# Optimization experiments

Measured on AMD Instinct MI355X. Metric: run time of the kernel, lower is better.

## Reference

```python
import jax, jax.numpy as jnp
import numpy as np


def conv3x3(x, w):
    # x: [B,C,H,W], w: [O,I,3,3], stride 1, pad 1, no bias
    return jax.lax.conv_general_dilated(
        x, w, window_strides=(1, 1), padding=[(1, 1), (1, 1)],
        dimension_numbers=("NCHW", "OIHW", "NCHW"))


def deform_conv2d(x, offset, w):
    """torchvision-style DeformConv2d: k=3, stride=1, pad=1, dilation=1,
    1 offset group, no bias. x:[B,C,H,W], offset:[B,18,H,W] (dy,dx pairs
    per kernel tap, k = kh*3+kw), w:[O,C,3,3]. Zero padding outside."""
    B, C, H, W = x.shape
    K = 9
    dy = offset[:, 0::2]  # [B,9,H,W]
    dx = offset[:, 1::2]
    kh = (jnp.arange(K) // 3 - 1).astype(x.dtype)[None, :, None, None]
    kw = (jnp.arange(K) % 3 - 1).astype(x.dtype)[None, :, None, None]
    hh = jnp.arange(H, dtype=x.dtype)[None, None, :, None]
    ww = jnp.arange(W, dtype=x.dtype)[None, None, None, :]
    py = hh + kh + dy  # sampling y coord, [B,9,H,W]
    px = ww + kw + dx
    y0 = jnp.floor(py)
    x0 = jnp.floor(px)
    wy = py - y0
    wx = px - x0
    x_hwc = jnp.transpose(x, (0, 2, 3, 1))  # [B,H,W,C]
    b_idx = jnp.arange(B)[:, None, None, None]

    def gather(yi, xi):
        valid = (yi >= 0) & (yi <= H - 1) & (xi >= 0) & (xi <= W - 1)
        yc = jnp.clip(yi, 0, H - 1).astype(jnp.int32)
        xc = jnp.clip(xi, 0, W - 1).astype(jnp.int32)
        v = x_hwc[b_idx, yc, xc]  # [B,9,H,W,C]
        return v * valid[..., None].astype(x.dtype)

    v00 = gather(y0, x0)
    v01 = gather(y0, x0 + 1)
    v10 = gather(y0 + 1, x0)
    v11 = gather(y0 + 1, x0 + 1)
    wy = wy[..., None]
    wx = wx[..., None]
    sampled = (v00 * (1 - wy) * (1 - wx) + v01 * (1 - wy) * wx
               + v10 * wy * (1 - wx) + v11 * wy * wx)  # [B,9,H,W,C]
    wk = w.reshape(w.shape[0], w.shape[1], K)  # [O,C,9]
    return jnp.einsum("bkhwc,ock->bohw", sampled, wk)


def setup_inputs() -> dict:
    key = jax.random.key(0)
    ks = jax.random.split(key, 6)
    B, C, H, W = 2, 128, 128, 128
    s = 0.05  # small init so learned offsets stay in a realistic range
    return {
        "input_features": jax.random.normal(ks[0], (B, C, H, W), jnp.float32),
        "reference_features": jax.random.normal(ks[1], (B, C, H, W), jnp.float32),
        "w_est1": jax.random.normal(ks[2], (C, 2 * C, 3, 3), jnp.float32) * s,
        "w_est2": jax.random.normal(ks[3], (C, C, 3, 3), jnp.float32) * s,
        "w_off": jax.random.normal(ks[4], (18, C, 3, 3), jnp.float32) * s,
        "w_def": jax.random.normal(ks[5], (C, C, 3, 3), jnp.float32) * s,
    }


def reference(input_features, reference_features, w_est1, w_est2, w_off, w_def):
    # concat input+reference features along channel dim
    feat = jnp.concatenate([input_features, reference_features], axis=1)  # [B,2C,H,W]
    # dynamic offset estimator: 2-layer 3x3 conv stack 2C->C->C with ReLU
    est = jax.nn.relu(conv3x3(feat, w_est1))
    est = jax.nn.relu(conv3x3(est, w_est2))
    # offset head: C -> 2*9 offsets per pixel
    offset = conv3x3(est, w_off)  # [B,18,H,W]
    # deformable conv over the reference features
    return deform_conv2d(reference_features, offset, w_def)
```

## Files before the change

kernel.cpp:

```cpp
#include <hip/hip_runtime.h>

typedef _Float16 f16;
typedef __attribute__((ext_vector_type(8))) _Float16 f16x8;
typedef __attribute__((ext_vector_type(4))) float f32x4;


__device__ __forceinline__ void g2l16(const void* g, void* l) {
  __builtin_amdgcn_global_load_lds((const __attribute__((address_space(1))) void*)g,
                                   (__attribute__((address_space(3))) void*)l, 16, 0, 0);
}

__device__ __forceinline__ void pack_conv(const float* __restrict__ src, f16* __restrict__ dst,
                                          long idx, int C) {
  int ci3 = idx & 7;
  int g = (idx >> 3) & 3;
  long t = idx >> 5;
  int o = (int)(t & 63); t >>= 6;
  int kx = (int)(t % 3); t /= 3;
  int nb = (int)(t & 1); t >>= 1;
  int nkc = C >> 5;
  int cc = (int)(t % nkc);
  int ky = (int)(t / nkc);
  int og = nb * 64 + o;
  int c = (cc << 5) + ((g ^ ((o >> 1) & 3)) << 3) + ci3;
  dst[idx] = (f16)src[(((size_t)og * C + c) * 3 + ky) * 3 + kx];
}

__device__ __forceinline__ void halo_zero(f16* __restrict__ buf, long e) {
  int c = (int)(e & 127);
  long t = e >> 7;
  int b = (int)(t / 516);
  int p = (int)(t % 516);
  int y, x;
  if (p < 130)      { y = 0;   x = p; }
  else if (p < 260) { y = 129; x = p - 130; }
  else if (p < 388) { x = 0;   y = p - 259; }
  else              { x = 129; y = p - 387; }
  buf[((size_t)(b * 130 + y) * 130 + x) * 128 + c] = (f16)0.f;
}

__global__ __launch_bounds__(256) void init_k(const float* __restrict__ x, const float* __restrict__ ref,
                                              const float* __restrict__ w1, const float* __restrict__ w2,
                                              const float* __restrict__ woff, const float* __restrict__ wdef,
                                              f16* __restrict__ W1p, f16* __restrict__ W2p,
                                              f16* __restrict__ Woffp, f16* __restrict__ Wdefp,
                                              f16* __restrict__ xP, f16* __restrict__ refP,
                                              f16* __restrict__ est1, f16* __restrict__ est2) {
  __shared__ __align__(16) f16 T[64][40];
  int tid = threadIdx.x;
  if (blockIdx.x < 4096) {
    int bi = blockIdx.x;
    int row = bi & 255, wseg = (bi >> 8) & 1, chunk = bi >> 9;
    int b = row >> 7, h = row & 127;
    int w0 = wseg * 64;
    const float* src = (chunk < 4) ? x : ref;
    f16* dstp = (chunk < 4) ? xP : refP;
    int c0 = (chunk & 3) * 32;
#pragma unroll
    for (int i = 0; i < 2; ++i) {
      int idx = tid + i * 256;
      int c = idx >> 4, g = idx & 15;
      const float4 v = *(const float4*)(src + (((size_t)(b * 128 + c0 + c)) * 128 + h) * 128 + w0 + g * 4);
      T[g * 4 + 0][c] = (f16)v.x;
      T[g * 4 + 1][c] = (f16)v.y;
      T[g * 4 + 2][c] = (f16)v.z;
      T[g * 4 + 3][c] = (f16)v.w;
    }
    __syncthreads();
    int w = tid >> 2, g = tid & 3;
    f16x8 o = *(const f16x8*)&T[w][g * 8];
    *(f16x8*)(dstp + ((size_t)(b * 130 + h + 1) * 130 + w0 + w + 1) * 128 + c0 + g * 8) = o;
    return;
  }
  long idx = (long)(blockIdx.x - 4096) * 256 + tid;
  if (idx < 294912) { pack_conv(w1, W1p, idx, 256); return; }
  idx -= 294912;
  if (idx < 147456) { pack_conv(w2, W2p, idx, 128); return; }
  idx -= 147456;
  if (idx < 36864) {
    int ci3 = (int)(idx & 7);
    int g = (int)((idx >> 3) & 3);
    int o = (int)((idx >> 5) & 31);
    int t2 = (int)(idx >> 10);
    int kx = t2 % 3; t2 /= 3;
    int cc = t2 & 3, ky = t2 >> 2;
    int c = (cc << 5) + ((g ^ ((o >> 1) & 3)) << 3) + ci3;
    Woffp[idx] = (o < 18) ? (f16)woff[(((size_t)o * 128 + c) * 3 + ky) * 3 + kx] : (f16)0.f;
    return;
  }
  idx -= 36864;
  if (idx < 147456) {
    int j = (int)(idx & 7);
    int ln = (int)((idx >> 3) & 63);
    int ofr = (int)((idx >> 9) & 7);
    int cc = (int)((idx >> 12) & 3);
    int t = (int)(idx >> 14);
    int o = ofr * 16 + (ln & 15);
    int c = cc * 32 + (ln >> 4) * 8 + j;
    Wdefp[idx] = (f16)wdef[(((size_t)o * 128 + c) * 3 + t / 3) * 3 + t % 3];
    return;
  }
  idx -= 147456;
  if (idx < 132096) { halo_zero(xP, idx); return; }
  idx -= 132096;
  if (idx < 132096) { halo_zero(refP, idx); return; }
  idx -= 132096;
  if (idx < 132096) { halo_zero(est1, idx); return; }
  idx -= 132096;
  if (idx < 132096) halo_zero(est2, idx);
}

template <int NKC>
__global__ __launch_bounds__(256, 3) void conv_k(const f16* __restrict__ src0,
                                                 const f16* __restrict__ src1,
                                                 const f16* __restrict__ Wp,
                                                 f16* __restrict__ dst) {
  constexpr int S = 3 * NKC;
  const int j = blockIdx.x;
  const int xcd = j & 7, ji = j >> 3;
  const int row = xcd * 32 + (ji & 31);
  const int nb = ji >> 5;
  const int b = row >> 7, h = row & 127;
  __shared__ __align__(16) f16 As[2][130][32];
  __shared__ __align__(16) f16 Bs[2][3][64][32];
  const int tid = threadIdx.x;
  const int lane = tid & 63, wave = tid >> 6;
  const int l16 = lane & 15, quad = lane >> 4;
  const int wmB = wave * 32;
  f32x4 acc[2][4] = {};

  auto stage = [&](int s, int buf) {
    int ky = s / NKC, cc = s % NKC;
    const f16* sp = (NKC == 8 && cc >= 4) ? src1 : src0;
    int c0 = (NKC == 8 ? (cc & 3) : cc) * 32;
    const f16* abase = sp + ((size_t)(b * 130 + h + ky) * 130) * 128 + c0;
#pragma unroll
    for (int rr = 0; rr < 2; ++rr) {
      int ch = rr * 256 + tid;
      int xx = ch >> 2, g = ch & 3;
      g2l16(abase + (size_t)xx * 128 + ((g ^ ((xx >> 1) & 3)) << 3),
            (char*)&As[buf][0][0] + ch * 16);
    }
    if (tid < 8) {
      int ch = 512 + tid;
      int xx = ch >> 2, g = ch & 3;
      g2l16(abase + (size_t)xx * 128 + ((g ^ ((xx >> 1) & 3)) << 3),
            (char*)&As[buf][0][0] + ch * 16);
    }
    const f16* bbase = Wp + (size_t)((ky * NKC + cc) * 2 + nb) * (3 * 64 * 32);
#pragma unroll
    for (int rr = 0; rr < 3; ++rr) {
      int ch = rr * 256 + tid;
      g2l16(bbase + (size_t)ch * 8, (char*)&Bs[buf][0][0][0] + ch * 16);
    }
  };

  stage(0, 0);
  __syncthreads();
  for (int s = 0; s < S; ++s) {
    if (s + 1 < S) stage(s + 1, (s + 1) & 1);
    const int buf = s & 1;
#pragma unroll
    for (int kx = 0; kx < 3; ++kx) {
      f16x8 bf[4];
#pragma unroll
      for (int j2 = 0; j2 < 4; ++j2) {
        int o = j2 * 16 + l16;
        bf[j2] = *(const f16x8*)&Bs[buf][kx][o][(quad ^ ((o >> 1) & 3)) << 3];
      }
#pragma unroll
      for (int i = 0; i < 2; ++i) {
        int xx = wmB + i * 16 + l16 + kx;
        f16x8 a = *(const f16x8*)&As[buf][xx][(quad ^ ((xx >> 1) & 3)) << 3];
#pragma unroll
        for (int j2 = 0; j2 < 4; ++j2)
          acc[i][j2] = __builtin_amdgcn_mfma_f32_16x16x32_f16(a, bf[j2], acc[i][j2], 0, 0, 0);
      }
    }
    __syncthreads();
  }
#pragma unroll
  for (int i = 0; i < 2; ++i)
#pragma unroll
    for (int j2 = 0; j2 < 4; ++j2) {
      int o = nb * 64 + j2 * 16 + l16;
#pragma unroll
      for (int rr = 0; rr < 4; ++rr) {
        int m = wmB + i * 16 + quad * 4 + rr;
        float v = fmaxf(acc[i][j2][rr], 0.f);
        dst[((size_t)(b * 130 + h + 1) * 130 + m + 1) * 128 + o] = (f16)v;
      }
    }
}

__global__ __launch_bounds__(256, 3) void conv_off_k(const f16* __restrict__ src,
                                                     const f16* __restrict__ Wp,
                                                     float* __restrict__ dst) {
  const int j = blockIdx.x;
  const int row = (j & 7) * 32 + (j >> 3);
  const int b = row >> 7, h = row & 127;
  __shared__ __align__(16) f16 As[2][130][32];
  __shared__ __align__(16) f16 Bs[2][3][32][32];
  const int tid = threadIdx.x;
  const int lane = tid & 63, wave = tid >> 6;
  const int l16 = lane & 15, quad = lane >> 4;
  const int wmB = wave * 32;
  f32x4 acc[2][2] = {};

  auto stage = [&](int s, int buf) {
    int ky = s >> 2, cc = s & 3;
    const f16* abase = src + ((size_t)(b * 130 + h + ky) * 130) * 128 + cc * 32;
#pragma unroll
    for (int rr = 0; rr < 2; ++rr) {
      int ch = rr * 256 + tid;
      int xx = ch >> 2, g = ch & 3;
      g2l16(abase + (size_t)xx * 128 + ((g ^ ((xx >> 1) & 3)) << 3),
            (char*)&As[buf][0][0] + ch * 16);
    }
    if (tid < 8) {
      int ch = 512 + tid;
      int xx = ch >> 2, g = ch & 3;
      g2l16(abase + (size_t)xx * 128 + ((g ^ ((xx >> 1) & 3)) << 3),
            (char*)&As[buf][0][0] + ch * 16);
    }
    const f16* bbase = Wp + (size_t)(ky * 4 + cc) * (3 * 32 * 32);
    {
      g2l16(bbase + (size_t)tid * 8, (char*)&Bs[buf][0][0][0] + tid * 16);
      if (tid < 128) {
        int ch = 256 + tid;
        g2l16(bbase + (size_t)ch * 8, (char*)&Bs[buf][0][0][0] + ch * 16);
      }
    }
  };

  stage(0, 0);
  __syncthreads();
  for (int s = 0; s < 12; ++s) {
    if (s + 1 < 12) stage(s + 1, (s + 1) & 1);
    const int buf = s & 1;
#pragma unroll
    for (int kx = 0; kx < 3; ++kx) {
      f16x8 bf[2];
#pragma unroll
      for (int j2 = 0; j2 < 2; ++j2) {
        int o = j2 * 16 + l16;
        bf[j2] = *(const f16x8*)&Bs[buf][kx][o][(quad ^ ((o >> 1) & 3)) << 3];
      }
#pragma unroll
      for (int i = 0; i < 2; ++i) {
        int xx = wmB + i * 16 + l16 + kx;
        f16x8 a = *(const f16x8*)&As[buf][xx][(quad ^ ((xx >> 1) & 3)) << 3];
#pragma unroll
        for (int j2 = 0; j2 < 2; ++j2)
          acc[i][j2] = __builtin_amdgcn_mfma_f32_16x16x32_f16(a, bf[j2], acc[i][j2], 0, 0, 0);
      }
    }
    __syncthreads();
  }
#pragma unroll
  for (int i = 0; i < 2; ++i)
#pragma unroll
    for (int j2 = 0; j2 < 2; ++j2)
#pragma unroll
      for (int rr = 0; rr < 4; ++rr) {
        int m = wmB + i * 16 + quad * 4 + rr;
        int o = j2 * 16 + l16;
        dst[((size_t)row * 128 + m) * 32 + o] = acc[i][j2][rr];
      }
}

__global__ __launch_bounds__(256, 3) void deform_k(const f16* __restrict__ refP,
                                                   const float* __restrict__ offb,
                                                   const f16* __restrict__ Wdefp,
                                                   float* __restrict__ out) {
  const int j = blockIdx.x;
  const int xcd = j & 7, ji = j >> 3;
  const int row = xcd * 32 + (ji & 31);
  const int tile = ji >> 5;
  const int b = row >> 7, h = row & 127;
  __shared__ __align__(16) f16 Ss[2][64][128];
  __shared__ int4 meta[9][64];
  const int tid = threadIdx.x;
  const int lane = tid & 63, wave = tid >> 6;
  const int l16 = lane & 15, quad = lane >> 4;

  for (int e = tid; e < 576; e += 256) {
    int t = e >> 6, p = e & 63;
    int wg = tile * 64 + p;
    const float2 d = *(const float2*)(offb + ((size_t)row * 128 + wg) * 32 + 2 * t);
    float py = (float)(h + t / 3 - 1) + d.x;
    float px = (float)(wg + t % 3 - 1) + d.y;
    float fy = floorf(py), fx = floorf(px);
    meta[t][p] = make_int4((int)fy, (int)fx, __float_as_int(py - fy), __float_as_int(px - fx));
  }

  auto sample = [&](int t, int buf) {
    const int p = tid >> 2, cg = tid & 3;
    int4 mt = meta[t][p];
    int yp = mt.x + 1, xp = mt.y + 1;
    float wy = __int_as_float(mt.z), wx = __int_as_float(mt.w);
    bool y0v = (unsigned)yp < 130u, y1v = (unsigned)(yp + 1) < 130u;
    bool x0v = (unsigned)xp < 130u, x1v = (unsigned)(xp + 1) < 130u;
    int cy0 = y0v ? yp : 0, cy1 = y1v ? yp + 1 : 0;
    int cx0 = x0v ? xp : 0, cx1 = x1v ? xp + 1 : 0;
    float u0 = (1.f - wy) * (y0v ? 1.f : 0.f), u1 = wy * (y1v ? 1.f : 0.f);
    float s0 = (1.f - wx) * (x0v ? 1.f : 0.f), s1 = wx * (x1v ? 1.f : 0.f);
    f16 h00 = (f16)(u0 * s0), h01 = (f16)(u0 * s1);
    f16 h10 = (f16)(u1 * s0), h11 = (f16)(u1 * s1);
    const size_t bb = (size_t)b * 130;
    const f16* p00 = refP + ((bb + cy0) * 130 + cx0) * 128 + cg * 32;
    const f16* p01 = refP + ((bb + cy0) * 130 + cx1) * 128 + cg * 32;
    const f16* p10 = refP + ((bb + cy1) * 130 + cx0) * 128 + cg * 32;
    const f16* p11 = refP + ((bb + cy1) * 130 + cx1) * 128 + cg * 32;
    f16x8 v00[4], v01[4], v10[4], v11[4];
#pragma unroll
    for (int q = 0; q < 4; ++q) {
      v00[q] = *(const f16x8*)(p00 + q * 8);
      v01[q] = *(const f16x8*)(p01 + q * 8);
      v10[q] = *(const f16x8*)(p10 + q * 8);
      v11[q] = *(const f16x8*)(p11 + q * 8);
    }
#pragma unroll
    for (int q = 0; q < 4; ++q) {
      f16x8 rb = v00[q] * h00 + v01[q] * h01 + v10[q] * h10 + v11[q] * h11;
      int c = cg * 4 + q;
      *(f16x8*)&Ss[buf][p][(c ^ (p & 7)) << 3] = rb;
    }
  };

  f32x4 acc[2][4] = {};
  __syncthreads();
  sample(0, 0);
  __syncthreads();
  for (int t = 0; t < 9; ++t) {
    f16x8 af[4][2];
#pragma unroll
    for (int cc = 0; cc < 4; ++cc)
#pragma unroll
      for (int i = 0; i < 2; ++i)
        af[cc][i] = *(const f16x8*)(Wdefp +
            ((((size_t)t * 4 + cc) * 8 + wave * 2 + i) * 64 + lane) * 8);
    if (t < 8) sample(t + 1, (t + 1) & 1);
    const int buf = t & 1;
#pragma unroll
    for (int cc = 0; cc < 4; ++cc) {
      f16x8 bf[4];
#pragma unroll
      for (int j2 = 0; j2 < 4; ++j2) {
        int p = j2 * 16 + l16;
        bf[j2] = *(const f16x8*)&Ss[buf][p][((cc * 4 + quad) ^ (p & 7)) << 3];
      }
#pragma unroll
      for (int i = 0; i < 2; ++i)
#pragma unroll
        for (int j2 = 0; j2 < 4; ++j2)
          acc[i][j2] = __builtin_amdgcn_mfma_f32_16x16x32_f16(af[cc][i], bf[j2], acc[i][j2], 0, 0, 0);
    }
    __syncthreads();
  }
#pragma unroll
  for (int i = 0; i < 2; ++i)
#pragma unroll
    for (int rr = 0; rr < 4; ++rr) {
      int o = wave * 32 + i * 16 + quad * 4 + rr;
#pragma unroll
      for (int j2 = 0; j2 < 4; ++j2) {
        int wg = tile * 64 + j2 * 16 + l16;
        out[((size_t)(b * 128 + o) * 128 + h) * 128 + wg] = acc[i][j2][rr];
      }
    }
}

extern "C" void kernel_launch(void* const* d_in, const int* in_sizes, int n_in,
                              void* d_out, int out_size, void* d_ws, size_t ws_size,
                              hipStream_t stream) {
  const float* x = (const float*)d_in[0];
  const float* ref = (const float*)d_in[1];
  const float* w1 = (const float*)d_in[2];
  const float* w2 = (const float*)d_in[3];
  const float* woff = (const float*)d_in[4];
  const float* wdef = (const float*)d_in[5];
  float* out = (float*)d_out;
  char* ws = (char*)d_ws;
  f16* xP = (f16*)(ws + 0);
  f16* refP = (f16*)(ws + 8652800);
  f16* est1 = (f16*)(ws + 17305600);
  f16* est2 = (f16*)(ws + 25958400);
  float* offb = (float*)(ws + 34611200);
  f16* W1p = (f16*)(ws + 38805504);
  f16* W2p = (f16*)(ws + 39395328);
  f16* Woffp = (f16*)(ws + 39690240);
  f16* Wdefp = (f16*)(ws + 39763968);

  init_k<<<dim3(8608), 256, 0, stream>>>(x, ref, w1, w2, woff, wdef,
                                         W1p, W2p, Woffp, Wdefp, xP, refP, est1, est2);
  conv_k<8><<<dim3(512), 256, 0, stream>>>(xP, refP, W1p, est1);
  conv_k<4><<<dim3(512), 256, 0, stream>>>(est1, est1, W2p, est2);
  conv_off_k<<<dim3(256), 256, 0, stream>>>(est2, Woffp, offb);
  deform_k<<<dim3(512), 256, 0, stream>>>(refP, offb, Wdefp, out);
}
```

Measured before the change: 169.1 us.

## Triple-buffer conv stages and split deform sampling into issue/finish around MFMAs

The conv kernels move from double to triple buffering in LDS. Each step waits with an explicit vmcnt for the older stage's async loads, then takes one barrier per step instead of two, so loads run two stages ahead. The deform kernel splits bilinear sampling into a load-issue phase before the MFMA loop and a blend/store phase after it, so gather latency overlaps the matrix math. Launch-bounds occupancy hints are lowered to fit the extra LDS and live registers, which risks lower occupancy. The hardcoded vmcnt values must match the exact number of loads issued per stage.

```diff
diff --git a/kernel.cpp b/kernel.cpp
--- a/kernel.cpp
+++ b/kernel.cpp
@@ -111,7 +111,7 @@
 }
 
 template <int NKC>
-__global__ __launch_bounds__(256, 3) void conv_k(const f16* __restrict__ src0,
+__global__ __launch_bounds__(256, 2) void conv_k(const f16* __restrict__ src0,
                                                  const f16* __restrict__ src1,
                                                  const f16* __restrict__ Wp,
                                                  f16* __restrict__ dst) {
@@ -121,8 +121,8 @@
   const int row = xcd * 32 + (ji & 31);
   const int nb = ji >> 5;
   const int b = row >> 7, h = row & 127;
-  __shared__ __align__(16) f16 As[2][130][32];
-  __shared__ __align__(16) f16 Bs[2][3][64][32];
+  __shared__ __align__(16) f16 As[3][130][32];
+  __shared__ __align__(16) f16 Bs[3][3][64][32];
   const int tid = threadIdx.x;
   const int lane = tid & 63, wave = tid >> 6;
   const int l16 = lane & 15, quad = lane >> 4;
@@ -156,28 +156,32 @@
   };
 
   stage(0, 0);
-  __syncthreads();
+  stage(1, 1);
+  int bc = 0, bn = 2;
   for (int s = 0; s < S; ++s) {
-    if (s + 1 < S) stage(s + 1, (s + 1) & 1);
-    const int buf = s & 1;
+    if (s + 1 < S) asm volatile("s_waitcnt vmcnt(5)" ::: "memory");
+    else           asm volatile("s_waitcnt vmcnt(0)" ::: "memory");
+    __builtin_amdgcn_s_barrier();
+    if (s + 2 < S) stage(s + 2, bn);
 #pragma unroll
     for (int kx = 0; kx < 3; ++kx) {
       f16x8 bf[4];
 #pragma unroll
       for (int j2 = 0; j2 < 4; ++j2) {
         int o = j2 * 16 + l16;
-        bf[j2] = *(const f16x8*)&Bs[buf][kx][o][(quad ^ ((o >> 1) & 3)) << 3];
+        bf[j2] = *(const f16x8*)&Bs[bc][kx][o][(quad ^ ((o >> 1) & 3)) << 3];
       }
 #pragma unroll
       for (int i = 0; i < 2; ++i) {
         int xx = wmB + i * 16 + l16 + kx;
-        f16x8 a = *(const f16x8*)&As[buf][xx][(quad ^ ((xx >> 1) & 3)) << 3];
+        f16x8 a = *(const f16x8*)&As[bc][xx][(quad ^ ((xx >> 1) & 3)) << 3];
 #pragma unroll
         for (int j2 = 0; j2 < 4; ++j2)
           acc[i][j2] = __builtin_amdgcn_mfma_f32_16x16x32_f16(a, bf[j2], acc[i][j2], 0, 0, 0);
       }
     }
-    __syncthreads();
+    bc = (bc == 2) ? 0 : bc + 1;
+    bn = (bn == 2) ? 0 : bn + 1;
   }
 #pragma unroll
   for (int i = 0; i < 2; ++i)
@@ -193,14 +197,14 @@
     }
 }
 
-__global__ __launch_bounds__(256, 3) void conv_off_k(const f16* __restrict__ src,
+__global__ __launch_bounds__(256, 1) void conv_off_k(const f16* __restrict__ src,
                                                      const f16* __restrict__ Wp,
                                                      float* __restrict__ dst) {
   const int j = blockIdx.x;
   const int row = (j & 7) * 32 + (j >> 3);
   const int b = row >> 7, h = row & 127;
-  __shared__ __align__(16) f16 As[2][130][32];
-  __shared__ __align__(16) f16 Bs[2][3][32][32];
+  __shared__ __align__(16) f16 As[3][130][32];
+  __shared__ __align__(16) f16 Bs[3][3][32][32];
   const int tid = threadIdx.x;
   const int lane = tid & 63, wave = tid >> 6;
   const int l16 = lane & 15, quad = lane >> 4;
@@ -234,28 +238,32 @@
   };
 
   stage(0, 0);
-  __syncthreads();
+  stage(1, 1);
+  int bc = 0, bn = 2;
   for (int s = 0; s < 12; ++s) {
-    if (s + 1 < 12) stage(s + 1, (s + 1) & 1);
-    const int buf = s & 1;
+    if (s + 1 < 12) asm volatile("s_waitcnt vmcnt(3)" ::: "memory");
+    else            asm volatile("s_waitcnt vmcnt(0)" ::: "memory");
+    __builtin_amdgcn_s_barrier();
+    if (s + 2 < 12) stage(s + 2, bn);
 #pragma unroll
     for (int kx = 0; kx < 3; ++kx) {
       f16x8 bf[2];
 #pragma unroll
       for (int j2 = 0; j2 < 2; ++j2) {
         int o = j2 * 16 + l16;
-        bf[j2] = *(const f16x8*)&Bs[buf][kx][o][(quad ^ ((o >> 1) & 3)) << 3];
+        bf[j2] = *(const f16x8*)&Bs[bc][kx][o][(quad ^ ((o >> 1) & 3)) << 3];
       }
 #pragma unroll
       for (int i = 0; i < 2; ++i) {
         int xx = wmB + i * 16 + l16 + kx;
-        f16x8 a = *(const f16x8*)&As[buf][xx][(quad ^ ((xx >> 1) & 3)) << 3];
+        f16x8 a = *(const f16x8*)&As[bc][xx][(quad ^ ((xx >> 1) & 3)) << 3];
 #pragma unroll
         for (int j2 = 0; j2 < 2; ++j2)
           acc[i][j2] = __builtin_amdgcn_mfma_f32_16x16x32_f16(a, bf[j2], acc[i][j2], 0, 0, 0);
       }
     }
-    __syncthreads();
+    bc = (bc == 2) ? 0 : bc + 1;
+    bn = (bn == 2) ? 0 : bn + 1;
   }
 #pragma unroll
   for (int i = 0; i < 2; ++i)
@@ -269,7 +277,7 @@
       }
 }
 
-__global__ __launch_bounds__(256, 3) void deform_k(const f16* __restrict__ refP,
+__global__ __launch_bounds__(256, 2) void deform_k(const f16* __restrict__ refP,
                                                    const float* __restrict__ offb,
                                                    const f16* __restrict__ Wdefp,
                                                    float* __restrict__ out) {
@@ -294,9 +302,12 @@
     meta[t][p] = make_int4((int)fy, (int)fx, __float_as_int(py - fy), __float_as_int(px - fx));
   }
 
-  auto sample = [&](int t, int buf) {
-    const int p = tid >> 2, cg = tid & 3;
-    int4 mt = meta[t][p];
+  const int sp_p = tid >> 2, sp_cg = tid & 3;
+  f16x8 v00[4], v01[4], v10[4], v11[4];
+  f16 h00, h01, h10, h11;
+
+  auto sample_issue = [&](int t) {
+    int4 mt = meta[t][sp_p];
     int yp = mt.x + 1, xp = mt.y + 1;
     float wy = __int_as_float(mt.z), wx = __int_as_float(mt.w);
     bool y0v = (unsigned)yp < 130u, y1v = (unsigned)(yp + 1) < 130u;
@@ -305,14 +316,13 @@
     int cx0 = x0v ? xp : 0, cx1 = x1v ? xp + 1 : 0;
     float u0 = (1.f - wy) * (y0v ? 1.f : 0.f), u1 = wy * (y1v ? 1.f : 0.f);
     float s0 = (1.f - wx) * (x0v ? 1.f : 0.f), s1 = wx * (x1v ? 1.f : 0.f);
-    f16 h00 = (f16)(u0 * s0), h01 = (f16)(u0 * s1);
-    f16 h10 = (f16)(u1 * s0), h11 = (f16)(u1 * s1);
+    h00 = (f16)(u0 * s0); h01 = (f16)(u0 * s1);
+    h10 = (f16)(u1 * s0); h11 = (f16)(u1 * s1);
     const size_t bb = (size_t)b * 130;
-    const f16* p00 = refP + ((bb + cy0) * 130 + cx0) * 128 + cg * 32;
-    const f16* p01 = refP + ((bb + cy0) * 130 + cx1) * 128 + cg * 32;
-    const f16* p10 = refP + ((bb + cy1) * 130 + cx0) * 128 + cg * 32;
-    const f16* p11 = refP + ((bb + cy1) * 130 + cx1) * 128 + cg * 32;
-    f16x8 v00[4], v01[4], v10[4], v11[4];
+    const f16* p00 = refP + ((bb + cy0) * 130 + cx0) * 128 + sp_cg * 32;
+    const f16* p01 = refP + ((bb + cy0) * 130 + cx1) * 128 + sp_cg * 32;
+    const f16* p10 = refP + ((bb + cy1) * 130 + cx0) * 128 + sp_cg * 32;
+    const f16* p11 = refP + ((bb + cy1) * 130 + cx1) * 128 + sp_cg * 32;
 #pragma unroll
     for (int q = 0; q < 4; ++q) {
       v00[q] = *(const f16x8*)(p00 + q * 8);
@@ -320,17 +330,20 @@
       v10[q] = *(const f16x8*)(p10 + q * 8);
       v11[q] = *(const f16x8*)(p11 + q * 8);
     }
+  };
+  auto sample_finish = [&](int buf) {
 #pragma unroll
     for (int q = 0; q < 4; ++q) {
       f16x8 rb = v00[q] * h00 + v01[q] * h01 + v10[q] * h10 + v11[q] * h11;
-      int c = cg * 4 + q;
-      *(f16x8*)&Ss[buf][p][(c ^ (p & 7)) << 3] = rb;
+      int c = sp_cg * 4 + q;
+      *(f16x8*)&Ss[buf][sp_p][(c ^ (sp_p & 7)) << 3] = rb;
     }
   };
 
   f32x4 acc[2][4] = {};
   __syncthreads();
-  sample(0, 0);
+  sample_issue(0);
+  sample_finish(0);
   __syncthreads();
   for (int t = 0; t < 9; ++t) {
     f16x8 af[4][2];
@@ -340,7 +353,7 @@
       for (int i = 0; i < 2; ++i)
         af[cc][i] = *(const f16x8*)(Wdefp +
             ((((size_t)t * 4 + cc) * 8 + wave * 2 + i) * 64 + lane) * 8);
-    if (t < 8) sample(t + 1, (t + 1) & 1);
+    if (t < 8) sample_issue(t + 1);
     const int buf = t & 1;
 #pragma unroll
     for (int cc = 0; cc < 4; ++cc) {
@@ -356,6 +369,7 @@
         for (int j2 = 0; j2 < 4; ++j2)
           acc[i][j2] = __builtin_amdgcn_mfma_f32_16x16x32_f16(af[cc][i], bf[j2], acc[i][j2], 0, 0, 0);
     }
+    if (t < 8) sample_finish((t + 1) & 1);
     __syncthreads();
   }
 #pragma unroll
```

Result: faster. 164.1 us (-3.0%).

## Stage conv tiles through registers and split deform sampling into issue/finish

Applied to the files above, without the earlier changes.

The conv kernels drop direct global-to-LDS loads. They now load the next-next stage into registers, write the next stage to LDS after compute, and add an extra barrier per step. The deformable sampler issues its bilinear gathers before the MFMA loop and blends and stores them afterward, so memory latency overlaps compute. Launch bounds drop from 3 to 2 blocks per SM to make room for the extra live registers, which lowers occupancy.

```diff
diff --git a/kernel.cpp b/kernel.cpp
--- a/kernel.cpp
+++ b/kernel.cpp
@@ -3,6 +3,7 @@
 typedef _Float16 f16;
 typedef __attribute__((ext_vector_type(8))) _Float16 f16x8;
 typedef __attribute__((ext_vector_type(4))) float f32x4;
+typedef __attribute__((ext_vector_type(4))) int i32x4;
 
 
 __device__ __forceinline__ void g2l16(const void* g, void* l) {
@@ -111,7 +112,7 @@
 }
 
 template <int NKC>
-__global__ __launch_bounds__(256, 3) void conv_k(const f16* __restrict__ src0,
+__global__ __launch_bounds__(256, 2) void conv_k(const f16* __restrict__ src0,
                                                  const f16* __restrict__ src1,
                                                  const f16* __restrict__ Wp,
                                                  f16* __restrict__ dst) {
@@ -129,36 +130,48 @@
   const int wmB = wave * 32;
   f32x4 acc[2][4] = {};
 
-  auto stage = [&](int s, int buf) {
+  i32x4 ra0, ra1, ra2, rb0, rb1, rb2;
+
+  auto stage_load = [&](int s) {
     int ky = s / NKC, cc = s % NKC;
     const f16* sp = (NKC == 8 && cc >= 4) ? src1 : src0;
     int c0 = (NKC == 8 ? (cc & 3) : cc) * 32;
     const f16* abase = sp + ((size_t)(b * 130 + h + ky) * 130) * 128 + c0;
-#pragma unroll
-    for (int rr = 0; rr < 2; ++rr) {
-      int ch = rr * 256 + tid;
-      int xx = ch >> 2, g = ch & 3;
-      g2l16(abase + (size_t)xx * 128 + ((g ^ ((xx >> 1) & 3)) << 3),
-            (char*)&As[buf][0][0] + ch * 16);
+    {
+      int ch = tid;
+      int xx = ch >> 2, g = ch & 3;
+      ra0 = *(const i32x4*)(abase + (size_t)xx * 128 + ((g ^ ((xx >> 1) & 3)) << 3));
+    }
+    {
+      int ch = 256 + tid;
+      int xx = ch >> 2, g = ch & 3;
+      ra1 = *(const i32x4*)(abase + (size_t)xx * 128 + ((g ^ ((xx >> 1) & 3)) << 3));
     }
     if (tid < 8) {
       int ch = 512 + tid;
       int xx = ch >> 2, g = ch & 3;
-      g2l16(abase + (size_t)xx * 128 + ((g ^ ((xx >> 1) & 3)) << 3),
-            (char*)&As[buf][0][0] + ch * 16);
+      ra2 = *(const i32x4*)(abase + (size_t)xx * 128 + ((g ^ ((xx >> 1) & 3)) << 3));
     }
     const f16* bbase = Wp + (size_t)((ky * NKC + cc) * 2 + nb) * (3 * 64 * 32);
-#pragma unroll
-    for (int rr = 0; rr < 3; ++rr) {
-      int ch = rr * 256 + tid;
-      g2l16(bbase + (size_t)ch * 8, (char*)&Bs[buf][0][0][0] + ch * 16);
-    }
-  };
-
-  stage(0, 0);
+    rb0 = *(const i32x4*)(bbase + (size_t)tid * 8);
+    rb1 = *(const i32x4*)(bbase + (size_t)(256 + tid) * 8);
+    rb2 = *(const i32x4*)(bbase + (size_t)(512 + tid) * 8);
+  };
+  auto stage_write = [&](int buf) {
+    *(i32x4*)((char*)&As[buf][0][0] + tid * 16) = ra0;
+    *(i32x4*)((char*)&As[buf][0][0] + (256 + tid) * 16) = ra1;
+    if (tid < 8)
+      *(i32x4*)((char*)&As[buf][0][0] + (512 + tid) * 16) = ra2;
+    *(i32x4*)((char*)&Bs[buf][0][0][0] + tid * 16) = rb0;
+    *(i32x4*)((char*)&Bs[buf][0][0][0] + (256 + tid) * 16) = rb1;
+    *(i32x4*)((char*)&Bs[buf][0][0][0] + (512 + tid) * 16) = rb2;
+  };
+
+  stage_load(0);
+  stage_write(0);
+  stage_load(1);
   __syncthreads();
   for (int s = 0; s < S; ++s) {
-    if (s + 1 < S) stage(s + 1, (s + 1) & 1);
     const int buf = s & 1;
 #pragma unroll
     for (int kx = 0; kx < 3; ++kx) {
@@ -177,6 +190,9 @@
           acc[i][j2] = __builtin_amdgcn_mfma_f32_16x16x32_f16(a, bf[j2], acc[i][j2], 0, 0, 0);
       }
     }
+    __syncthreads();
+    if (s + 1 < S) stage_write((s + 1) & 1);
+    if (s + 2 < S) stage_load(s + 2);
     __syncthreads();
   }
 #pragma unroll
@@ -193,7 +209,7 @@
     }
 }
 
-__global__ __launch_bounds__(256, 3) void conv_off_k(const f16* __restrict__ src,
+__global__ __launch_bounds__(256, 2) void conv_off_k(const f16* __restrict__ src,
                                                      const f16* __restrict__ Wp,
                                                      float* __restrict__ dst) {
   const int j = blockIdx.x;
@@ -207,36 +223,45 @@
   const int wmB = wave * 32;
   f32x4 acc[2][2] = {};
 
-  auto stage = [&](int s, int buf) {
+  i32x4 ra0, ra1, ra2, rb0, rb1;
+
+  auto stage_load = [&](int s) {
     int ky = s >> 2, cc = s & 3;
     const f16* abase = src + ((size_t)(b * 130 + h + ky) * 130) * 128 + cc * 32;
-#pragma unroll
-    for (int rr = 0; rr < 2; ++rr) {
-      int ch = rr * 256 + tid;
-      int xx = ch >> 2, g = ch & 3;
-      g2l16(abase + (size_t)xx * 128 + ((g ^ ((xx >> 1) & 3)) << 3),
-            (char*)&As[buf][0][0] + ch * 16);
+    {
+      int ch = tid;
+      int xx = ch >> 2, g = ch & 3;
+      ra0 = *(const i32x4*)(abase + (size_t)xx * 128 + ((g ^ ((xx >> 1) & 3)) << 3));
+    }
+    {
+      int ch = 256 + tid;
+      int xx = ch >> 2, g = ch & 3;
+      ra1 = *(const i32x4*)(abase + (size_t)xx * 128 + ((g ^ ((xx >> 1) & 3)) << 3));
     }
     if (tid < 8) {
       int ch = 512 + tid;
       int xx = ch >> 2, g = ch & 3;
-      g2l16(abase + (size_t)xx * 128 + ((g ^ ((xx >> 1) & 3)) << 3),
-            (char*)&As[buf][0][0] + ch * 16);
+      ra2 = *(const i32x4*)(abase + (size_t)xx * 128 + ((g ^ ((xx >> 1) & 3)) << 3));
     }
     const f16* bbase = Wp + (size_t)(ky * 4 + cc) * (3 * 32 * 32);
-    {
-      g2l16(bbase + (size_t)tid * 8, (char*)&Bs[buf][0][0][0] + tid * 16);
-      if (tid < 128) {
-        int ch = 256 + tid;
-        g2l16(bbase + (size_t)ch * 8, (char*)&Bs[buf][0][0][0] + ch * 16);
-      }
-    }
-  };
-
-  stage(0, 0);
+    rb0 = *(const i32x4*)(bbase + (size_t)tid * 8);
+    if (tid < 128) rb1 = *(const i32x4*)(bbase + (size_t)(256 + tid) * 8);
+  };
+  auto stage_write = [&](int buf) {
+    *(i32x4*)((char*)&As[buf][0][0] + tid * 16) = ra0;
+    *(i32x4*)((char*)&As[buf][0][0] + (256 + tid) * 16) = ra1;
+    if (tid < 8)
+      *(i32x4*)((char*)&As[buf][0][0] + (512 + tid) * 16) = ra2;
+    *(i32x4*)((char*)&Bs[buf][0][0][0] + tid * 16) = rb0;
+    if (tid < 128)
+      *(i32x4*)((char*)&Bs[buf][0][0][0] + (256 + tid) * 16) = rb1;
+  };
+
+  stage_load(0);
+  stage_write(0);
+  stage_load(1);
   __syncthreads();
   for (int s = 0; s < 12; ++s) {
-    if (s + 1 < 12) stage(s + 1, (s + 1) & 1);
     const int buf = s & 1;
 #pragma unroll
     for (int kx = 0; kx < 3; ++kx) {
@@ -255,6 +280,9 @@
           acc[i][j2] = __builtin_amdgcn_mfma_f32_16x16x32_f16(a, bf[j2], acc[i][j2], 0, 0, 0);
       }
     }
+    __syncthreads();
+    if (s + 1 < 12) stage_write((s + 1) & 1);
+    if (s + 2 < 12) stage_load(s + 2);
     __syncthreads();
   }
 #pragma unroll
@@ -269,7 +297,7 @@
       }
 }
 
-__global__ __launch_bounds__(256, 3) void deform_k(const f16* __restrict__ refP,
+__global__ __launch_bounds__(256, 2) void deform_k(const f16* __restrict__ refP,
                                                    const float* __restrict__ offb,
                                                    const f16* __restrict__ Wdefp,
                                                    float* __restrict__ out) {
@@ -294,9 +322,12 @@
     meta[t][p] = make_int4((int)fy, (int)fx, __float_as_int(py - fy), __float_as_int(px - fx));
   }
 
-  auto sample = [&](int t, int buf) {
-    const int p = tid >> 2, cg = tid & 3;
-    int4 mt = meta[t][p];
+  const int sp_p = tid >> 2, sp_cg = tid & 3;
+  f16x8 v00[4], v01[4], v10[4], v11[4];
+  f16 h00, h01, h10, h11;
+
+  auto sample_issue = [&](int t) {
+    int4 mt = meta[t][sp_p];
     int yp = mt.x + 1, xp = mt.y + 1;
     float wy = __int_as_float(mt.z), wx = __int_as_float(mt.w);
     bool y0v = (unsigned)yp < 130u, y1v = (unsigned)(yp + 1) < 130u;
@@ -305,14 +336,13 @@
     int cx0 = x0v ? xp : 0, cx1 = x1v ? xp + 1 : 0;
     float u0 = (1.f - wy) * (y0v ? 1.f : 0.f), u1 = wy * (y1v ? 1.f : 0.f);
     float s0 = (1.f - wx) * (x0v ? 1.f : 0.f), s1 = wx * (x1v ? 1.f : 0.f);
-    f16 h00 = (f16)(u0 * s0), h01 = (f16)(u0 * s1);
-    f16 h10 = (f16)(u1 * s0), h11 = (f16)(u1 * s1);
+    h00 = (f16)(u0 * s0); h01 = (f16)(u0 * s1);
+    h10 = (f16)(u1 * s0); h11 = (f16)(u1 * s1);
     const size_t bb = (size_t)b * 130;
-    const f16* p00 = refP + ((bb + cy0) * 130 + cx0) * 128 + cg * 32;
-    const f16* p01 = refP + ((bb + cy0) * 130 + cx1) * 128 + cg * 32;
-    const f16* p10 = refP + ((bb + cy1) * 130 + cx0) * 128 + cg * 32;
-    const f16* p11 = refP + ((bb + cy1) * 130 + cx1) * 128 + cg * 32;
-    f16x8 v00[4], v01[4], v10[4], v11[4];
+    const f16* p00 = refP + ((bb + cy0) * 130 + cx0) * 128 + sp_cg * 32;
+    const f16* p01 = refP + ((bb + cy0) * 130 + cx1) * 128 + sp_cg * 32;
+    const f16* p10 = refP + ((bb + cy1) * 130 + cx0) * 128 + sp_cg * 32;
+    const f16* p11 = refP + ((bb + cy1) * 130 + cx1) * 128 + sp_cg * 32;
 #pragma unroll
     for (int q = 0; q < 4; ++q) {
       v00[q] = *(const f16x8*)(p00 + q * 8);
@@ -320,17 +350,20 @@
       v10[q] = *(const f16x8*)(p10 + q * 8);
       v11[q] = *(const f16x8*)(p11 + q * 8);
     }
+  };
+  auto sample_finish = [&](int buf) {
 #pragma unroll
     for (int q = 0; q < 4; ++q) {
       f16x8 rb = v00[q] * h00 + v01[q] * h01 + v10[q] * h10 + v11[q] * h11;
-      int c = cg * 4 + q;
-      *(f16x8*)&Ss[buf][p][(c ^ (p & 7)) << 3] = rb;
+      int c = sp_cg * 4 + q;
+      *(f16x8*)&Ss[buf][sp_p][(c ^ (sp_p & 7)) << 3] = rb;
     }
   };
 
   f32x4 acc[2][4] = {};
   __syncthreads();
-  sample(0, 0);
+  sample_issue(0);
+  sample_finish(0);
   __syncthreads();
   for (int t = 0; t < 9; ++t) {
     f16x8 af[4][2];
@@ -340,7 +373,7 @@
       for (int i = 0; i < 2; ++i)
         af[cc][i] = *(const f16x8*)(Wdefp +
             ((((size_t)t * 4 + cc) * 8 + wave * 2 + i) * 64 + lane) * 8);
-    if (t < 8) sample(t + 1, (t + 1) & 1);
+    if (t < 8) sample_issue(t + 1);
     const int buf = t & 1;
 #pragma unroll
     for (int cc = 0; cc < 4; ++cc) {
@@ -356,6 +389,7 @@
         for (int j2 = 0; j2 < 4; ++j2)
           acc[i][j2] = __builtin_amdgcn_mfma_f32_16x16x32_f16(af[cc][i], bf[j2], acc[i][j2], 0, 0, 0);
     }
+    if (t < 8) sample_finish((t + 1) & 1);
     __syncthreads();
   }
 #pragma unroll
```

Result: faster. 161.3 us (-4.6%).
